# Optimization experiments

Hardware: AMD Instinct MI355X
Metric: run time of the kernel (lower is better)

## Reference

```python
import jax, jax.numpy as jnp
import numpy as np

H = 31  # hidden_size == input_size


def setup_inputs() -> dict:
    key = jax.random.key(0)
    ks = jax.random.split(key, 7)
    B, T = 2048, 512
    s = 1.0 / np.sqrt(H)
    return {
        "x": jax.random.normal(ks[0], (B, T, H), dtype=jnp.float32),
        "W_ih": jax.random.uniform(ks[1], (3 * H, H), minval=-s, maxval=s, dtype=jnp.float32),
        "W_hh": jax.random.uniform(ks[2], (3 * H, H), minval=-s, maxval=s, dtype=jnp.float32),
        "b_ih": jax.random.uniform(ks[3], (3 * H,), minval=-s, maxval=s, dtype=jnp.float32),
        "b_hh": jax.random.uniform(ks[4], (3 * H,), minval=-s, maxval=s, dtype=jnp.float32),
        "W_fc": jax.random.uniform(ks[5], (2, H), minval=-s, maxval=s, dtype=jnp.float32),
        "b_fc": jax.random.uniform(ks[6], (2,), minval=-s, maxval=s, dtype=jnp.float32),
    }


def _gru_seq(x, W_ih, W_hh, b_ih, b_hh):
    # x: [B, T, I]. Precompute input-side gates for all timesteps (one big GEMM).
    B = x.shape[0]
    xg = jnp.einsum("bti,gi->btg", x, W_ih) + b_ih          # [B, T, 3H]
    xg = jnp.swapaxes(xg, 0, 1)                              # [T, B, 3H]

    def step(h, xg_t):
        gh = h @ W_hh.T + b_hh                               # [B, 3H]
        ir, iz, inn = jnp.split(xg_t, 3, axis=-1)
        hr, hz, hn = jnp.split(gh, 3, axis=-1)
        r = jax.nn.sigmoid(ir + hr)
        z = jax.nn.sigmoid(iz + hz)
        n = jnp.tanh(inn + r * hn)
        h_new = (1.0 - z) * n + z * h
        return h_new, h_new

    h0 = jnp.zeros((B, H), dtype=x.dtype)
    _, out = jax.lax.scan(step, h0, xg)                      # out: [T, B, H]
    return jnp.swapaxes(out, 0, 1)                           # [B, T, H]


def reference(x, W_ih, W_hh, b_ih, b_hh, W_fc, b_fc):
    out = _gru_seq(x, W_ih, W_hh, b_ih, b_hh)                # [B, T, H]
    return out @ W_fc.T + b_fc                               # [B, T, 2]
```

## Files before the change

### kernel.cpp

```cpp
#include <hip/hip_runtime.h>


constexpr int BB = 2048, TT = 512, HH = 31;

typedef _Float16 hf2 __attribute__((ext_vector_type(2)));

__device__ __forceinline__ float dot2(int pk, hf2 w, float acc) {
#if __has_builtin(__builtin_amdgcn_fdot2)
    return __builtin_amdgcn_fdot2(__builtin_bit_cast(hf2, pk), w, acc, false);
#else
    hf2 a = __builtin_bit_cast(hf2, pk);
    return acc + (float)a.x * (float)w.x + (float)a.y * (float)w.y;
#endif
}

__global__ __launch_bounds__(64, 1) void gru_pair_kernel(
    const float* __restrict__ x, const float* __restrict__ W_ih,
    const float* __restrict__ W_hh, const float* __restrict__ b_ih,
    const float* __restrict__ b_hh, const float* __restrict__ W_fc,
    const float* __restrict__ b_fc, float* __restrict__ out)
{
    __shared__ _Float16 hbuf[2][32];
    __shared__ _Float16 xbuf[2][2][32];

    const int lane = threadIdx.x & 63;
    const int li   = lane & 31;
    const int half = lane >> 5;
    const int b    = blockIdx.x * 2 + half;
    const bool unit = (li < HH);

    const float* ph0 = unit ? W_hh + (size_t)li * HH            : W_fc;
    const float* ph1 = unit ? W_hh + (size_t)(HH + li) * HH     : W_fc + HH;
    const float* ph2 = unit ? W_hh + (size_t)(2 * HH + li) * HH : nullptr;
    const float* px0 = unit ? W_ih + (size_t)li * HH            : nullptr;
    const float* px1 = unit ? W_ih + (size_t)(HH + li) * HH     : nullptr;
    const float* px2 = unit ? W_ih + (size_t)(2 * HH + li) * HH : nullptr;

    hf2 wh0[16], wh1[16], wh2[16], wx0[16], wx1[16], wx2[16];
#pragma unroll
    for (int m = 0; m < 16; ++m) {
        auto pk = [&](const float* p) -> hf2 {
            hf2 r;
            r.x = p ? (_Float16)p[2 * m] : (_Float16)0.f;
            r.y = (p && (2 * m + 1) < HH) ? (_Float16)p[2 * m + 1] : (_Float16)0.f;
            return r;
        };
        wh0[m] = pk(ph0); wh1[m] = pk(ph1); wh2[m] = pk(ph2);
        wx0[m] = pk(px0); wx1[m] = pk(px1); wx2[m] = pk(px2);
    }

    float arH0, azH0, anH0, anX0;
    if (unit) {
        arH0 = b_ih[li] + b_hh[li];
        azH0 = b_ih[HH + li] + b_hh[HH + li];
        anH0 = b_hh[2 * HH + li];
        anX0 = b_ih[2 * HH + li];
    } else {
        arH0 = b_fc[0]; azH0 = b_fc[1]; anH0 = 0.f; anX0 = 0.f;
    }

    const float* xb   = x + (size_t)b * TT * HH;
    float*       outb = out + (size_t)b * TT * 2;

    hbuf[half][li]    = (_Float16)0.f;
    xbuf[0][half][li] = unit ? (_Float16)xb[li]      : (_Float16)0.f;
    xbuf[1][half][li] = unit ? (_Float16)xb[HH + li] : (_Float16)0.f;
    float xpre = unit ? xb[(size_t)2 * HH + li] : 0.f;
    float hval = 0.f;

    const int4* HP  = (const int4*)(&hbuf[half][0]);
    const int4* XB0 = (const int4*)(&xbuf[0][half][0]);
    const int4* XB1 = (const int4*)(&xbuf[1][half][0]);

    int4 xq0 = XB0[0], xq1 = XB0[1], xq2 = XB0[2], xq3 = XB0[3];

#pragma unroll 2
    for (int t = 0; t < TT; ++t) {
        int4 hq0 = HP[0], hq1 = HP[1], hq2 = HP[2], hq3 = HP[3];

        float arH = arH0, azH = azH0, anH = anH0;
        float arX = 0.f, azX = 0.f, anX = anX0;
#define STEPM(m, hp, xp) \
        arH = dot2(hp, wh0[m], arH); azH = dot2(hp, wh1[m], azH); \
        anH = dot2(hp, wh2[m], anH); arX = dot2(xp, wx0[m], arX); \
        azX = dot2(xp, wx1[m], azX); anX = dot2(xp, wx2[m], anX);
        STEPM(0,  hq0.x, xq0.x) STEPM(1,  hq0.y, xq0.y)
        STEPM(2,  hq0.z, xq0.z) STEPM(3,  hq0.w, xq0.w)
        STEPM(4,  hq1.x, xq1.x) STEPM(5,  hq1.y, xq1.y)
        STEPM(6,  hq1.z, xq1.z) STEPM(7,  hq1.w, xq1.w)
        STEPM(8,  hq2.x, xq2.x) STEPM(9,  hq2.y, xq2.y)
        STEPM(10, hq2.z, xq2.z) STEPM(11, hq2.w, xq2.w)
        STEPM(12, hq3.x, xq3.x) STEPM(13, hq3.y, xq3.y)
        STEPM(14, hq3.z, xq3.z) STEPM(15, hq3.w, xq3.w)
#undef STEPM

        const float sumr = arH + arX;
        const float sumz = azH + azX;
        if (li == 31 && t > 0)
            *(float2*)(outb + (size_t)(t - 1) * 2) = make_float2(sumr, sumz);

        const float r    = __fdividef(1.f, 1.f + __expf(-sumr));
        const float z    = __fdividef(1.f, 1.f + __expf(-sumz));
        const float npre = fmaf(r, anH, anX);
        const float nn   = __fdividef(2.f, 1.f + __expf(-2.f * npre)) - 1.f;
        const float hnew = nn + z * (hval - nn);
        hval = unit ? hnew : 0.f;
        hbuf[half][li] = (_Float16)hval;

        xbuf[t & 1][half][li] = unit ? (_Float16)xpre : (_Float16)0.f;
        int tn = t + 3; if (tn > TT - 1) tn = TT - 1;
        xpre = unit ? xb[(size_t)tn * HH + li] : 0.f;

        const int4* XN = (t & 1) ? XB0 : XB1;
        xq0 = XN[0]; xq1 = XN[1]; xq2 = XN[2]; xq3 = XN[3];
    }

    {
        int4 hq0 = HP[0], hq1 = HP[1], hq2 = HP[2], hq3 = HP[3];
        float f0 = arH0, f1 = azH0;
#define FST(m, hp) f0 = dot2(hp, wh0[m], f0); f1 = dot2(hp, wh1[m], f1);
        FST(0,  hq0.x) FST(1,  hq0.y) FST(2,  hq0.z) FST(3,  hq0.w)
        FST(4,  hq1.x) FST(5,  hq1.y) FST(6,  hq1.z) FST(7,  hq1.w)
        FST(8,  hq2.x) FST(9,  hq2.y) FST(10, hq2.z) FST(11, hq2.w)
        FST(12, hq3.x) FST(13, hq3.y) FST(14, hq3.z) FST(15, hq3.w)
#undef FST
        if (li == 31)
            *(float2*)(outb + (size_t)(TT - 1) * 2) = make_float2(f0, f1);
    }
}

extern "C" void kernel_launch(void* const* d_in, const int* in_sizes, int n_in,
                              void* d_out, int out_size, void* d_ws, size_t ws_size,
                              hipStream_t stream) {
    const float* x    = (const float*)d_in[0];
    const float* W_ih = (const float*)d_in[1];
    const float* W_hh = (const float*)d_in[2];
    const float* b_ih = (const float*)d_in[3];
    const float* b_hh = (const float*)d_in[4];
    const float* W_fc = (const float*)d_in[5];
    const float* b_fc = (const float*)d_in[6];
    float* out = (float*)d_out;

    dim3 grid(BB / 2);
    dim3 block(64);
    gru_pair_kernel<<<grid, block, 0, stream>>>(x, W_ih, W_hh, b_ih, b_hh,
                                                W_fc, b_fc, out);
}
```

Baseline: 283.9 us.

## Split GRU into fp16 input-gate GEMM pass plus lighter recurrent kernel

Adds a separate pass that packs W_ih to fp16 and computes all input-side gate preactivations into a workspace buffer in fp16, laid out per batch, row and time. The recurrent kernel then only does the W_hh dot products. Each batch's gate rows are split across the two half-waves, partial sums are exchanged with lane shuffles, and the precomputed gates are prefetched in 8-step chunks. This takes the x·W_ih work off the serial critical path, but adds a large workspace write and read of about 200 MB plus extra launches. The old single kernel remains as a fallback when the workspace is too small.

```diff
diff --git a/kernel.cpp b/kernel.cpp
--- a/kernel.cpp
+++ b/kernel.cpp
@@ -2,16 +2,187 @@
 
 
 constexpr int BB = 2048, TT = 512, HH = 31;
+constexpr int RR = 96;
+constexpr size_t XG_BYTES = (size_t)BB * RR * TT * 2;
+constexpr int WPAIRS = 93 * 16;
+constexpr size_t WS_NEEDED = XG_BYTES + (size_t)WPAIRS * 4;
+
+#define MEMFENCE asm volatile("" ::: "memory")
 
 typedef _Float16 hf2 __attribute__((ext_vector_type(2)));
 
-__device__ __forceinline__ float dot2(int pk, hf2 w, float acc) {
+__device__ __forceinline__ float dot2(int a, hf2 w, float acc) {
 #if __has_builtin(__builtin_amdgcn_fdot2)
-    return __builtin_amdgcn_fdot2(__builtin_bit_cast(hf2, pk), w, acc, false);
+    return __builtin_amdgcn_fdot2(__builtin_bit_cast(hf2, a), w, acc, false);
 #else
-    hf2 a = __builtin_bit_cast(hf2, pk);
-    return acc + (float)a.x * (float)w.x + (float)a.y * (float)w.y;
+    hf2 x = __builtin_bit_cast(hf2, a);
+    return acc + (float)x.x * (float)w.x + (float)x.y * (float)w.y;
 #endif
+}
+
+__global__ void pack_wih_kernel(const float* __restrict__ W_ih, int* __restrict__ wpk) {
+    int q = blockIdx.x * blockDim.x + threadIdx.x;
+    if (q >= WPAIRS) return;
+    int row = q >> 4, p = q & 15;
+    float lo = W_ih[row * HH + 2 * p];
+    float hi = (2 * p + 1 < HH) ? W_ih[row * HH + 2 * p + 1] : 0.f;
+    hf2 w; w.x = (_Float16)lo; w.y = (_Float16)hi;
+    wpk[q] = __builtin_bit_cast(int, w);
+}
+
+__global__ __launch_bounds__(128, 2) void xg_gemm_kernel(
+    const float* __restrict__ x, const int* __restrict__ wpk,
+    const float* __restrict__ b_ih, _Float16* __restrict__ xg)
+{
+    const int tid = threadIdx.x;
+    const int b   = blockIdx.x;
+    const int t0  = tid * 4;
+    const float* xb = x + ((size_t)b * TT + t0) * HH;
+
+    hf2 xp[4][16];
+#pragma unroll
+    for (int j = 0; j < 4; ++j)
+#pragma unroll
+        for (int p = 0; p < 16; ++p) {
+            float lo = xb[j * HH + 2 * p];
+            float hi = (2 * p + 1 < HH) ? xb[j * HH + 2 * p + 1] : 0.f;
+            xp[j][p].x = (_Float16)lo; xp[j][p].y = (_Float16)hi;
+        }
+
+    _Float16* xgb = xg + (size_t)b * RR * TT + t0;
+    for (int row = 0; row < 93; ++row) {
+        const float bi = b_ih[row];
+        float a0 = bi, a1 = bi, a2 = bi, a3 = bi;
+        const int* wr = wpk + row * 16;
+#pragma unroll
+        for (int p = 0; p < 16; ++p) {
+            const int w = wr[p];
+            a0 = dot2(w, xp[0][p], a0);
+            a1 = dot2(w, xp[1][p], a1);
+            a2 = dot2(w, xp[2][p], a2);
+            a3 = dot2(w, xp[3][p], a3);
+        }
+        hf2 lo2; lo2.x = (_Float16)a0; lo2.y = (_Float16)a1;
+        hf2 hi2; hi2.x = (_Float16)a2; hi2.y = (_Float16)a3;
+        *reinterpret_cast<int2*>(xgb + (size_t)row * TT) =
+            make_int2(__builtin_bit_cast(int, lo2), __builtin_bit_cast(int, hi2));
+    }
+    for (int row = 93; row < 96; ++row)
+        *reinterpret_cast<int2*>(xgb + (size_t)row * TT) = make_int2(0, 0);
+}
+
+__global__ __launch_bounds__(256, 2) void gru_rec_kernel(
+    const _Float16* __restrict__ xg, const float* __restrict__ W_hh,
+    const float* __restrict__ b_hh, const float* __restrict__ W_fc,
+    const float* __restrict__ b_fc, float* __restrict__ out)
+{
+    __shared__ _Float16 hbuf[4][32];
+    const int tid = threadIdx.x, wv = tid >> 6, lane = tid & 63;
+    const int li = lane & 31, half = lane >> 5;
+    const int b  = blockIdx.x * 4 + wv;
+    const bool u = (li < HH);
+
+    const float* pA = u ? W_hh + (size_t)(half * HH + li) * HH : W_fc + half * HH;
+    const float* pN = W_hh + (size_t)(2 * HH + (u ? li : 0)) * HH;
+    const float bA0 = u ? b_hh[half * HH + li] : b_fc[half];
+    const float bN0 = (u && half == 0) ? b_hh[2 * HH + li] : 0.f;
+
+    hf2 wA[16], wN[8];
+#pragma unroll
+    for (int p = 0; p < 16; ++p) {
+        const int pp = (p + 8 * half) & 15;
+        float lo = pA[2 * pp];
+        float hi = (2 * pp + 1 < HH) ? pA[2 * pp + 1] : 0.f;
+        wA[p].x = (_Float16)lo; wA[p].y = (_Float16)hi;
+    }
+#pragma unroll
+    for (int p = 0; p < 8; ++p) {
+        const int pp = 8 * half + p;
+        float lo = u ? pN[2 * pp] : 0.f;
+        float hi = (u && 2 * pp + 1 < HH) ? pN[2 * pp + 1] : 0.f;
+        wN[p].x = (_Float16)lo; wN[p].y = (_Float16)hi;
+    }
+
+    const int rowA = u ? half * HH + li : 93 + half;
+    const int rowN = u ? 2 * HH + li : 95;
+    const _Float16* gA = xg + ((size_t)b * RR + rowA) * TT;
+    const _Float16* gN = xg + ((size_t)b * RR + rowN) * TT;
+    float* outb = out + (size_t)b * TT * 2;
+
+    if (half == 0) hbuf[wv][li] = (_Float16)0.f;
+    MEMFENCE;
+
+    const int4* HP = (const int4*)&hbuf[wv][0];
+    const int i0 = (0 + 2 * half) & 3, i1 = (1 + 2 * half) & 3,
+              i2 = (2 + 2 * half) & 3, i3 = (3 + 2 * half) & 3;
+
+    int4 bufA = *(const int4*)gA;
+    int4 bufN = *(const int4*)gN;
+    float hval = 0.f;
+
+    for (int tb = 0; tb < TT / 8; ++tb) {
+        int4 nxtA = bufA, nxtN = bufN;
+        if (tb + 1 < TT / 8) {
+            nxtA = *(const int4*)(gA + (size_t)(tb + 1) * 8);
+            nxtN = *(const int4*)(gN + (size_t)(tb + 1) * 8);
+        }
+#pragma unroll
+        for (int s = 0; s < 8; ++s) {
+            const int t = tb * 8 + s;
+            const int4 h0 = HP[i0], h1 = HP[i1], h2 = HP[i2], h3 = HP[i3];
+            const float xa = (float)(((const _Float16*)&bufA)[s]);
+            const float xn = (float)(((const _Float16*)&bufN)[s]);
+
+            float n0 = bN0, n1 = 0.f;
+            n0 = dot2(h0.x, wN[0], n0); n1 = dot2(h0.y, wN[1], n1);
+            n0 = dot2(h0.z, wN[2], n0); n1 = dot2(h0.w, wN[3], n1);
+            n0 = dot2(h1.x, wN[4], n0); n1 = dot2(h1.y, wN[5], n1);
+            n0 = dot2(h1.z, wN[6], n0); n1 = dot2(h1.w, wN[7], n1);
+            const float accN = n0 + n1;
+            const float nsw = __shfl_xor(accN, 32);
+
+            float a0v = bA0 + xa, a1v = 0.f;
+            a0v = dot2(h0.x, wA[0], a0v);  a1v = dot2(h0.y, wA[1], a1v);
+            a0v = dot2(h0.z, wA[2], a0v);  a1v = dot2(h0.w, wA[3], a1v);
+            a0v = dot2(h1.x, wA[4], a0v);  a1v = dot2(h1.y, wA[5], a1v);
+            a0v = dot2(h1.z, wA[6], a0v);  a1v = dot2(h1.w, wA[7], a1v);
+            a0v = dot2(h2.x, wA[8], a0v);  a1v = dot2(h2.y, wA[9], a1v);
+            a0v = dot2(h2.z, wA[10], a0v); a1v = dot2(h2.w, wA[11], a1v);
+            a0v = dot2(h3.x, wA[12], a0v); a1v = dot2(h3.y, wA[13], a1v);
+            a0v = dot2(h3.z, wA[14], a0v); a1v = dot2(h3.w, wA[15], a1v);
+            const float accA = a0v + a1v;
+            const float asw = __shfl_xor(accA, 32);
+
+            if (li == 31 && t > 0) outb[(size_t)(t - 1) * 2 + half] = accA;
+
+            const float g  = __fdividef(1.f, 1.f + __expf(-accA));
+            const float go = __fdividef(1.f, 1.f + __expf(-asw));
+            const float r = half ? go : g;
+            const float z = half ? g  : go;
+            const float nh   = accN + nsw;
+            const float npre = fmaf(r, nh, xn);
+            const float nn   = __fdividef(2.f, 1.f + __expf(-2.f * npre)) - 1.f;
+            const float hnew = nn + z * (hval - nn);
+            hval = u ? hnew : 0.f;
+            if (half == 0) hbuf[wv][li] = (_Float16)hval;
+            MEMFENCE;
+        }
+        bufA = nxtA; bufN = nxtN;
+    }
+
+    {
+        const int4 h0 = HP[i0], h1 = HP[i1], h2 = HP[i2], h3 = HP[i3];
+        float a0v = bA0, a1v = 0.f;
+        a0v = dot2(h0.x, wA[0], a0v);  a1v = dot2(h0.y, wA[1], a1v);
+        a0v = dot2(h0.z, wA[2], a0v);  a1v = dot2(h0.w, wA[3], a1v);
+        a0v = dot2(h1.x, wA[4], a0v);  a1v = dot2(h1.y, wA[5], a1v);
+        a0v = dot2(h1.z, wA[6], a0v);  a1v = dot2(h1.w, wA[7], a1v);
+        a0v = dot2(h2.x, wA[8], a0v);  a1v = dot2(h2.y, wA[9], a1v);
+        a0v = dot2(h2.z, wA[10], a0v); a1v = dot2(h2.w, wA[11], a1v);
+        a0v = dot2(h3.x, wA[12], a0v); a1v = dot2(h3.y, wA[13], a1v);
+        a0v = dot2(h3.z, wA[14], a0v); a1v = dot2(h3.w, wA[15], a1v);
+        if (li == 31) outb[(size_t)(TT - 1) * 2 + half] = a0v + a1v;
+    }
 }
 
 __global__ __launch_bounds__(64, 1) void gru_pair_kernel(
@@ -65,6 +236,7 @@
     hbuf[half][li]    = (_Float16)0.f;
     xbuf[0][half][li] = unit ? (_Float16)xb[li]      : (_Float16)0.f;
     xbuf[1][half][li] = unit ? (_Float16)xb[HH + li] : (_Float16)0.f;
+    MEMFENCE;
     float xpre = unit ? xb[(size_t)2 * HH + li] : 0.f;
     float hval = 0.f;
 
@@ -96,7 +268,7 @@
 
         const float sumr = arH + arX;
         const float sumz = azH + azX;
-        if (li == 31 && t > 0)
+        if (lane == 31 && t > 0)
             *(float2*)(outb + (size_t)(t - 1) * 2) = make_float2(sumr, sumz);
 
         const float r    = __fdividef(1.f, 1.f + __expf(-sumr));
@@ -108,6 +280,7 @@
         hbuf[half][li] = (_Float16)hval;
 
         xbuf[t & 1][half][li] = unit ? (_Float16)xpre : (_Float16)0.f;
+        MEMFENCE;
         int tn = t + 3; if (tn > TT - 1) tn = TT - 1;
         xpre = unit ? xb[(size_t)tn * HH + li] : 0.f;
 
@@ -124,7 +297,7 @@
         FST(8,  hq2.x) FST(9,  hq2.y) FST(10, hq2.z) FST(11, hq2.w)
         FST(12, hq3.x) FST(13, hq3.y) FST(14, hq3.z) FST(15, hq3.w)
 #undef FST
-        if (li == 31)
+        if (lane == 31)
             *(float2*)(outb + (size_t)(TT - 1) * 2) = make_float2(f0, f1);
     }
 }
@@ -141,8 +314,14 @@
     const float* b_fc = (const float*)d_in[6];
     float* out = (float*)d_out;
 
-    dim3 grid(BB / 2);
-    dim3 block(64);
-    gru_pair_kernel<<<grid, block, 0, stream>>>(x, W_ih, W_hh, b_ih, b_hh,
-                                                W_fc, b_fc, out);
-}
+    if (ws_size >= WS_NEEDED) {
+        _Float16* xg = (_Float16*)d_ws;
+        int* wpk = (int*)((char*)d_ws + XG_BYTES);
+        pack_wih_kernel<<<(WPAIRS + 255) / 256, 256, 0, stream>>>(W_ih, wpk);
+        xg_gemm_kernel<<<BB, 128, 0, stream>>>(x, wpk, b_ih, xg);
+        gru_rec_kernel<<<BB / 4, 256, 0, stream>>>(xg, W_hh, b_hh, W_fc, b_fc, out);
+    } else {
+        gru_pair_kernel<<<BB / 2, 64, 0, stream>>>(x, W_ih, W_hh, b_ih, b_hh,
+                                                   W_fc, b_fc, out);
+    }
+}
```

Result: slower. 301.4 us (+6.2%).
